# Performance work log

Hardware: AMD Instinct MI355X
Metric: run time of the kernel (lower is better)

The kernel has to match this reference:

```python
import jax, jax.numpy as jnp
import numpy as np

D = 1024
H = 16
K = 32768
EPS = 1e-5


def setup_inputs() -> dict:
    key = jax.random.key(0)
    ks = jax.random.split(key, 12)
    s = 1.0 / np.sqrt(D)
    return {
        "query": jax.random.normal(ks[0], (D,), jnp.float32),
        "neighbors": jax.random.normal(ks[1], (K, D), jnp.float32),
        # nn.MultiheadAttention params
        "in_proj_w": jax.random.uniform(ks[2], (3 * D, D), jnp.float32, -s, s),
        "in_proj_b": jnp.zeros((3 * D,), jnp.float32),
        "out_proj_w": jax.random.uniform(ks[3], (D, D), jnp.float32, -s, s),
        "out_proj_b": jnp.zeros((D,), jnp.float32),
        # FFN params
        "w1": jax.random.uniform(ks[4], (4 * D, D), jnp.float32, -s, s),
        "b1": jnp.zeros((4 * D,), jnp.float32),
        "w2": jax.random.uniform(ks[5], (D, 4 * D), jnp.float32, -s, s),
        "b2": jnp.zeros((D,), jnp.float32),
        # LayerNorm params
        "g1": jnp.ones((D,), jnp.float32),
        "be1": jnp.zeros((D,), jnp.float32),
        "g2": jnp.ones((D,), jnp.float32),
        "be2": jnp.zeros((D,), jnp.float32),
    }


def _layernorm(x, g, b):
    m = jnp.mean(x, axis=-1, keepdims=True)
    v = jnp.var(x, axis=-1, keepdims=True)
    return (x - m) * jax.lax.rsqrt(v + EPS) * g + b


def reference(query, neighbors, in_proj_w, in_proj_b, out_proj_w, out_proj_b,
              w1, b1, w2, b2, g1, be1, g2, be2):
    dh = D // H
    wq, wk, wv = in_proj_w[:D], in_proj_w[D:2 * D], in_proj_w[2 * D:]
    bq, bk, bv = in_proj_b[:D], in_proj_b[D:2 * D], in_proj_b[2 * D:]

    q = (query @ wq.T + bq).reshape(H, dh)            # [H, dh]
    k = (neighbors @ wk.T + bk).reshape(K, H, dh)     # [K, H, dh]
    v = (neighbors @ wv.T + bv).reshape(K, H, dh)

    scores = jnp.einsum('hd,khd->hk', q, k) / np.sqrt(dh)  # [H, K]
    attn = jax.nn.softmax(scores, axis=-1)
    ctx = jnp.einsum('hk,khd->hd', attn, v).reshape(D)      # [D]
    attn_out = ctx @ out_proj_w.T + out_proj_b

    x = _layernorm(query + attn_out, g1, be1)
    ffn = jax.nn.gelu(x @ w1.T + b1, approximate=False) @ w2.T + b2
    return _layernorm(x + ffn, g2, be2)
```

## Files before the change

### kernel.cpp

```cpp
#include <hip/hip_runtime.h>
#include <hip/hip_bf16.h>

#define D 1024
#define H 16
#define DH 64
#define KN 32768
#define EPS 1e-5f

__device__ __forceinline__ float wave_sum(float v){
  #pragma unroll
  for (int off = 32; off; off >>= 1) v += __shfl_xor(v, off, 64);
  return v;
}

#define GLL(gp, lp) __builtin_amdgcn_global_load_lds((const __attribute__((address_space(1))) void*)(gp), (__attribute__((address_space(3))) void*)(lp), 16, 0, 0)

__global__ void g_qproj(const float* __restrict__ query, const float* __restrict__ ipw,
                        const float* __restrict__ ipb, float* __restrict__ q){
  int j = blockIdx.x, l = threadIdx.x;
  const float4* qv = (const float4*)(query + l*16);
  const float4* wv = (const float4*)(ipw + (size_t)j*D + l*16);
  float acc = 0.f;
  #pragma unroll
  for (int t = 0; t < 4; t++){
    float4 a = qv[t], b = wv[t];
    acc += a.x*b.x + a.y*b.y + a.z*b.z + a.w*b.w;
  }
  acc = wave_sum(acc);
  if (l == 0) q[j] = acc + ipb[j];
}

__global__ __launch_bounds__(256) void g_qk(const float* __restrict__ ipw, const float* __restrict__ ipb,
                                            const float* __restrict__ q, float* __restrict__ qk,
                                            float* __restrict__ sb){
  int b = blockIdx.x, t = threadIdx.x;
  int h = b >> 2, sl = b & 3;
  int jg = t >> 6, c = t & 63;
  __shared__ float qh[DH];
  __shared__ float4 red[256];
  if (t < DH) qh[t] = q[h*DH + t];
  __syncthreads();
  if (t < DH){
    float p = qh[t] * ipb[D + h*DH + t];
    p = wave_sum(p);
    if (t == 0 && sl == 0) sb[h] = p;
  }
  float4 acc = make_float4(0.f,0.f,0.f,0.f);
  for (int jj = 0; jj < 16; jj++){
    int j = jg*16 + jj;
    float4 w = *((const float4*)(ipw + (size_t)(D + h*DH + j)*D) + sl*64 + c);
    float qj = qh[j];
    acc.x += qj*w.x; acc.y += qj*w.y; acc.z += qj*w.z; acc.w += qj*w.w;
  }
  red[t] = acc;
  __syncthreads();
  if (jg == 0){
    float4 a = red[c], b1 = red[64+c], c1 = red[128+c], d1 = red[192+c];
    float4 r = make_float4(a.x+b1.x+c1.x+d1.x, a.y+b1.y+c1.y+d1.y,
                           a.z+b1.z+c1.z+d1.z, a.w+b1.w+c1.w+d1.w);
    ((float4*)(qk + h*D))[sl*64 + c] = r;
  }
}

__global__ void g_attn(const float* __restrict__ nbr, const float* __restrict__ qk,
                       const float* __restrict__ sb, float* __restrict__ lpart,
                       float* __restrict__ part, int rows_per_blk){
  __shared__ __align__(16) float tile[2][8*D];
  int t = threadIdx.x;
  int h = t >> 6, ci = t & 63;
  int wb = t & ~63;
  float sbh = sb[h];

  float qkv[16];
  {
    const float4* qp = (const float4*)(qk + h*D);
    #pragma unroll
    for (int c = 0; c < 4; c++){
      float4 f = qp[c*64 + ci];
      qkv[4*c]=f.x; qkv[4*c+1]=f.y; qkv[4*c+2]=f.z; qkv[4*c+3]=f.w;
    }
  }
  float acc[16];
  #pragma unroll
  for (int i = 0; i < 16; i++) acc[i] = 0.f;
  float lsum = 0.f;

  const int k0 = blockIdx.x * rows_per_blk;
  const int ntiles = rows_per_blk >> 3;
  const uint4* gb = (const uint4*)nbr;

  {
    const uint4* g = gb + (size_t)k0*256;
    #pragma unroll
    for (int i = 0; i < 2; i++) GLL(g + i*1024 + t, &tile[0][(i*1024 + wb)*4]);
  }
  __syncthreads();

  #pragma unroll 1
  for (int tl = 0; tl < ntiles; tl++){
    int cur = tl & 1;
    if (tl + 1 < ntiles){
      const uint4* g = gb + (size_t)(k0 + (tl+1)*8)*256;
      #pragma unroll
      for (int i = 0; i < 2; i++) GLL(g + i*1024 + t, &tile[cur^1][(i*1024 + wb)*4]);
    }
    #pragma unroll 1
    for (int r = 0; r < 8; r++){
      const float4* row4 = (const float4*)(tile[cur]) + r*256;
      float xf[16];
      float s = 0.f;
      #pragma unroll
      for (int c = 0; c < 4; c++){
        float4 a = row4[c*64 + ci];
        xf[4*c]=a.x; xf[4*c+1]=a.y; xf[4*c+2]=a.z; xf[4*c+3]=a.w;
        s += a.x*qkv[4*c] + a.y*qkv[4*c+1] + a.z*qkv[4*c+2] + a.w*qkv[4*c+3];
      }
      s = wave_sum(s);
      float p = __expf((s + sbh)*0.125f);
      lsum += p;
      #pragma unroll
      for (int i = 0; i < 16; i++) acc[i] += p*xf[i];
    }
    __syncthreads();
  }

  if (ci == 0) lpart[blockIdx.x*H + h] = lsum;
  float4* o = (float4*)(part + (size_t)blockIdx.x*(H*D) + h*D);
  #pragma unroll
  for (int c = 0; c < 4; c++)
    o[c*64 + ci] = make_float4(acc[4*c], acc[4*c+1], acc[4*c+2], acc[4*c+3]);
}

__global__ __launch_bounds__(256) void g_red(const float* __restrict__ part, const float* __restrict__ lpart,
                                             float* __restrict__ nb, float* __restrict__ lh, int nblk){
  int b = blockIdx.x, t = threadIdx.x;
  if (b == 64){
    if (t < H){
      float s = 0.f;
      for (int c = 0; c < nblk; c++) s += lpart[c*H + t];
      lh[t] = s;
    }
    return;
  }
  int o = b*256 + t;
  float s = 0.f;
  #pragma unroll 8
  for (int c = 0; c < nblk; c++) s += part[(size_t)c*(H*D) + o];
  nb[o] = s;
}

__global__ void g_ctx(const float* __restrict__ ipw, const float* __restrict__ ipb,
                      const float* __restrict__ nb, const float* __restrict__ lh,
                      float* __restrict__ ctx){
  int j = blockIdx.x, l = threadIdx.x, h = j >> 6;
  const float4* wv = (const float4*)(ipw + (size_t)(2*D + j)*D + l*16);
  const float4* nv = (const float4*)(nb + h*D + l*16);
  float acc = 0.f;
  #pragma unroll
  for (int t = 0; t < 4; t++){
    float4 b = wv[t], n = nv[t];
    acc += b.x*n.x + b.y*n.y + b.z*n.z + b.w*n.w;
  }
  acc = wave_sum(acc);
  if (l == 0) ctx[j] = acc/lh[h] + ipb[2*D + j];
}

__global__ void g_attnout(const float* __restrict__ opw, const float* __restrict__ opb,
                          const float* __restrict__ query, const float* __restrict__ ctx,
                          float* __restrict__ xb){
  int j = blockIdx.x, l = threadIdx.x;
  const float4* wv = (const float4*)(opw + (size_t)j*D + l*16);
  const float4* cv = (const float4*)(ctx + l*16);
  float acc = 0.f;
  #pragma unroll
  for (int t = 0; t < 4; t++){
    float4 b = wv[t], c = cv[t];
    acc += b.x*c.x + b.y*c.y + b.z*c.z + b.w*c.w;
  }
  acc = wave_sum(acc);
  if (l == 0) xb[j] = query[j] + acc + opb[j];
}

__global__ __launch_bounds__(256) void g_ffn1(const float* __restrict__ w1, const float* __restrict__ b1,
                                              const float* __restrict__ xb,
                                              const float* __restrict__ g1, const float* __restrict__ be1,
                                              float* __restrict__ xln, float* __restrict__ h1){
  int t = threadIdx.x, b = blockIdx.x;
  __shared__ float xs[D];
  __shared__ float red[8];
  float4 v = ((const float4*)xb)[t];
  float s = wave_sum(v.x + v.y + v.z + v.w);
  if ((t & 63) == 0) red[t >> 6] = s;
  __syncthreads();
  float m = (red[0]+red[1]+red[2]+red[3]) * (1.0f/D);
  float4 d = make_float4(v.x-m, v.y-m, v.z-m, v.w-m);
  float s2 = wave_sum(d.x*d.x + d.y*d.y + d.z*d.z + d.w*d.w);
  if ((t & 63) == 0) red[4 + (t >> 6)] = s2;
  __syncthreads();
  float var = (red[4]+red[5]+red[6]+red[7]) * (1.0f/D);
  float rs = rsqrtf(var + EPS);
  float4 gg = ((const float4*)g1)[t], bb = ((const float4*)be1)[t];
  float4 r = make_float4(d.x*rs*gg.x + bb.x, d.y*rs*gg.y + bb.y,
                         d.z*rs*gg.z + bb.z, d.w*rs*gg.w + bb.w);
  ((float4*)xs)[t] = r;
  if (b == 0) ((float4*)xln)[t] = r;
  __syncthreads();

  int w = t >> 6, l = t & 63;
  const float4* xs4 = (const float4*)xs;
  #pragma unroll 1
  for (int rr = 0; rr < 4; rr++){
    int j = b*16 + w*4 + rr;
    const float4* wr = (const float4*)(w1 + (size_t)j*D);
    float a = 0.f;
    #pragma unroll
    for (int c = 0; c < 4; c++){
      float4 ww = wr[c*64 + l], xx = xs4[c*64 + l];
      a += ww.x*xx.x + ww.y*xx.y + ww.z*xx.z + ww.w*xx.w;
    }
    a = wave_sum(a);
    if (l == 0){
      float z = a + b1[j];
      h1[j] = 0.5f*z*(1.0f + erff(z*0.70710678118654752f));
    }
  }
}

__global__ void g_ffn2(const float* __restrict__ w2, const float* __restrict__ b2v,
                       const float* __restrict__ h1, float* __restrict__ y){
  int j = blockIdx.x, l = threadIdx.x;
  const float4* wv = (const float4*)(w2 + (size_t)j*4096 + l*64);
  const float4* hv = (const float4*)(h1 + l*64);
  float acc = 0.f;
  #pragma unroll
  for (int t = 0; t < 16; t++){
    float4 b = wv[t], hh = hv[t];
    acc += b.x*hh.x + b.y*hh.y + b.z*hh.z + b.w*hh.w;
  }
  acc = wave_sum(acc);
  if (l == 0) y[j] = acc + b2v[j];
}

__global__ __launch_bounds__(1024) void g_ln2(const float* __restrict__ xln, const float* __restrict__ y,
                                              const float* __restrict__ g, const float* __restrict__ be,
                                              float* __restrict__ out){
  int t = threadIdx.x;
  __shared__ float red[16];
  __shared__ float bc;
  float v = xln[t] + y[t];
  float s = wave_sum(v);
  if ((t & 63) == 0) red[t >> 6] = s;
  __syncthreads();
  if (t == 0){ float a = 0.f; for (int i = 0; i < 16; i++) a += red[i]; bc = a*(1.0f/D); }
  __syncthreads();
  float m = bc;
  float d = v - m;
  float s2 = wave_sum(d*d);
  if ((t & 63) == 0) red[t >> 6] = s2;
  __syncthreads();
  if (t == 0){ float a = 0.f; for (int i = 0; i < 16; i++) a += red[i]; bc = a*(1.0f/D); }
  __syncthreads();
  float rs = rsqrtf(bc + EPS);
  out[t] = d*rs*g[t] + be[t];
}

extern "C" void kernel_launch(void* const* d_in, const int* in_sizes, int n_in,
                              void* d_out, int out_size, void* d_ws, size_t ws_size,
                              hipStream_t stream) {
  const float* query = (const float*)d_in[0];
  const float* nbr   = (const float*)d_in[1];
  const float* ipw   = (const float*)d_in[2];
  const float* ipb   = (const float*)d_in[3];
  const float* opw   = (const float*)d_in[4];
  const float* opb   = (const float*)d_in[5];
  const float* w1    = (const float*)d_in[6];
  const float* b1    = (const float*)d_in[7];
  const float* w2    = (const float*)d_in[8];
  const float* b2v   = (const float*)d_in[9];
  const float* g1    = (const float*)d_in[10];
  const float* be1   = (const float*)d_in[11];
  const float* g2    = (const float*)d_in[12];
  const float* be2   = (const float*)d_in[13];

  float* ws    = (float*)d_ws;
  float* q     = ws;
  float* qk    = q + D;
  float* sb    = qk + H*D;
  float* lh    = sb + 16;
  float* ctx   = lh + 16;
  float* xb    = ctx + D;
  float* xln   = xb + D;
  float* h1    = xln + D;
  float* y     = h1 + 4*D;
  float* nb    = y + D;
  float* lpart = nb + H*D;
  float* part  = lpart + 4096;

  size_t fixed_bytes = (size_t)(part - ws) * 4;
  int nblk = 256;
  while (nblk > 32 && fixed_bytes + (size_t)nblk*H*D*4 > ws_size) nblk >>= 1;
  int rows_per_blk = KN / nblk;

  g_qproj  <<<1024, 64, 0, stream>>>(query, ipw, ipb, q);
  g_qk     <<<64, 256, 0, stream>>>(ipw, ipb, q, qk, sb);
  g_attn   <<<nblk, 1024, 0, stream>>>(nbr, qk, sb, lpart, part, rows_per_blk);
  g_red    <<<65, 256, 0, stream>>>(part, lpart, nb, lh, nblk);
  g_ctx    <<<1024, 64, 0, stream>>>(ipw, ipb, nb, lh, ctx);
  g_attnout<<<1024, 64, 0, stream>>>(opw, opb, query, ctx, xb);
  g_ffn1   <<<256, 256, 0, stream>>>(w1, b1, xb, g1, be1, xln, h1);
  g_ffn2   <<<1024, 64, 0, stream>>>(w2, b2v, h1, y);
  g_ln2    <<<1, 1024, 0, stream>>>(xln, y, g2, be2, (float*)d_out);
}
```

Measured before the change: 348.2 us.

## Fuse all stages into one persistent kernel with software grid barriers

```diff
diff --git a/kernel.cpp b/kernel.cpp
--- a/kernel.cpp
+++ b/kernel.cpp
@@ -3,9 +3,24 @@
 
 #define D 1024
 #define H 16
-#define DH 64
 #define KN 32768
 #define EPS 1e-5f
+#define NB 256
+#define RPB 128
+
+#define O_Q     0
+#define O_QK    1024
+#define O_SB    17408
+#define O_LH    17424
+#define O_CTX   17440
+#define O_XB    18464
+#define O_XLN   19488
+#define O_H1    20512
+#define O_Y     24608
+#define O_NBUF  25632
+#define O_LPART 42016
+#define O_BAR   46112
+#define O_PART  46176
 
 __device__ __forceinline__ float wave_sum(float v){
   #pragma unroll
@@ -15,203 +30,253 @@
 
 #define GLL(gp, lp) __builtin_amdgcn_global_load_lds((const __attribute__((address_space(1))) void*)(gp), (__attribute__((address_space(3))) void*)(lp), 16, 0, 0)
 
-__global__ void g_qproj(const float* __restrict__ query, const float* __restrict__ ipw,
-                        const float* __restrict__ ipb, float* __restrict__ q){
-  int j = blockIdx.x, l = threadIdx.x;
-  const float4* qv = (const float4*)(query + l*16);
-  const float4* wv = (const float4*)(ipw + (size_t)j*D + l*16);
-  float acc = 0.f;
-  #pragma unroll
-  for (int t = 0; t < 4; t++){
-    float4 a = qv[t], b = wv[t];
-    acc += a.x*b.x + a.y*b.y + a.z*b.z + a.w*b.w;
-  }
-  acc = wave_sum(acc);
-  if (l == 0) q[j] = acc + ipb[j];
-}
-
-__global__ __launch_bounds__(256) void g_qk(const float* __restrict__ ipw, const float* __restrict__ ipb,
-                                            const float* __restrict__ q, float* __restrict__ qk,
-                                            float* __restrict__ sb){
-  int b = blockIdx.x, t = threadIdx.x;
-  int h = b >> 2, sl = b & 3;
-  int jg = t >> 6, c = t & 63;
-  __shared__ float qh[DH];
-  __shared__ float4 red[256];
-  if (t < DH) qh[t] = q[h*DH + t];
+__device__ __forceinline__ void gbar(int* bar, int idx){
   __syncthreads();
-  if (t < DH){
-    float p = qh[t] * ipb[D + h*DH + t];
-    p = wave_sum(p);
-    if (t == 0 && sl == 0) sb[h] = p;
-  }
-  float4 acc = make_float4(0.f,0.f,0.f,0.f);
-  for (int jj = 0; jj < 16; jj++){
-    int j = jg*16 + jj;
-    float4 w = *((const float4*)(ipw + (size_t)(D + h*DH + j)*D) + sl*64 + c);
-    float qj = qh[j];
-    acc.x += qj*w.x; acc.y += qj*w.y; acc.z += qj*w.z; acc.w += qj*w.w;
-  }
-  red[t] = acc;
+  if (threadIdx.x == 0){
+    int* cnt = bar + idx*2;
+    int* gen = bar + idx*2 + 1;
+    __threadfence();
+    int g = atomicAdd(gen, 0);
+    if (atomicAdd(cnt, 1) == (int)gridDim.x - 1){
+      atomicExch(cnt, 0);
+      atomicAdd(gen, 1);
+    } else {
+      while (atomicAdd(gen, 0) == g){ __builtin_amdgcn_s_sleep(2); }
+    }
+    __threadfence();
+  }
   __syncthreads();
-  if (jg == 0){
-    float4 a = red[c], b1 = red[64+c], c1 = red[128+c], d1 = red[192+c];
-    float4 r = make_float4(a.x+b1.x+c1.x+d1.x, a.y+b1.y+c1.y+d1.y,
-                           a.z+b1.z+c1.z+d1.z, a.w+b1.w+c1.w+d1.w);
-    ((float4*)(qk + h*D))[sl*64 + c] = r;
-  }
-}
-
-__global__ void g_attn(const float* __restrict__ nbr, const float* __restrict__ qk,
-                       const float* __restrict__ sb, float* __restrict__ lpart,
-                       float* __restrict__ part, int rows_per_blk){
+}
+
+__global__ void g_init(int* bar){
+  if (threadIdx.x < 64) bar[threadIdx.x] = 0;
+}
+
+__global__ __launch_bounds__(1024) void g_fused(
+    const float* __restrict__ query, const float* __restrict__ nbr,
+    const float* __restrict__ ipw,   const float* __restrict__ ipb,
+    const float* __restrict__ opw,   const float* __restrict__ opb,
+    const float* __restrict__ w1,    const float* __restrict__ b1,
+    const float* __restrict__ w2,    const float* __restrict__ b2v,
+    const float* __restrict__ g1,    const float* __restrict__ be1,
+    const float* __restrict__ g2,    const float* __restrict__ be2,
+    float* __restrict__ ws, float* __restrict__ out){
+
+  float* q     = ws + O_Q;
+  float* qk    = ws + O_QK;
+  float* sb    = ws + O_SB;
+  float* lh    = ws + O_LH;
+  float* ctx   = ws + O_CTX;
+  float* xb    = ws + O_XB;
+  float* xln   = ws + O_XLN;
+  float* h1    = ws + O_H1;
+  float* y     = ws + O_Y;
+  float* nbuf  = ws + O_NBUF;
+  float* lpart = ws + O_LPART;
+  int*   bar   = (int*)(ws + O_BAR);
+  float* part  = ws + O_PART;
+
   __shared__ __align__(16) float tile[2][8*D];
-  int t = threadIdx.x;
-  int h = t >> 6, ci = t & 63;
-  int wb = t & ~63;
-  float sbh = sb[h];
-
-  float qkv[16];
+  __shared__ float smem[1056];
+  float* xs  = smem;
+  float* red = smem + 1024;
+  float* bcs = smem + 1040;
+
+  const int b = blockIdx.x, t = threadIdx.x;
+  const int w = t >> 6, l = t & 63;
+
+  if (w < 4){
+    int j = b*4 + w;
+    const float4* qv = (const float4*)(query + l*16);
+    const float4* wv = (const float4*)(ipw + (size_t)j*D + l*16);
+    float a = 0.f;
+    #pragma unroll
+    for (int c = 0; c < 4; c++){
+      float4 aa = qv[c], bb = wv[c];
+      a += aa.x*bb.x + aa.y*bb.y + aa.z*bb.z + aa.w*bb.w;
+    }
+    a = wave_sum(a);
+    if (l == 0) q[j] = a + ipb[j];
+  }
+  gbar(bar, 0);
+
   {
-    const float4* qp = (const float4*)(qk + h*D);
-    #pragma unroll
-    for (int c = 0; c < 4; c++){
-      float4 f = qp[c*64 + ci];
-      qkv[4*c]=f.x; qkv[4*c+1]=f.y; qkv[4*c+2]=f.z; qkv[4*c+3]=f.w;
-    }
-  }
-  float acc[16];
-  #pragma unroll
-  for (int i = 0; i < 16; i++) acc[i] = 0.f;
-  float lsum = 0.f;
-
-  const int k0 = blockIdx.x * rows_per_blk;
-  const int ntiles = rows_per_blk >> 3;
-  const uint4* gb = (const uint4*)nbr;
-
-  {
-    const uint4* g = gb + (size_t)k0*256;
-    #pragma unroll
-    for (int i = 0; i < 2; i++) GLL(g + i*1024 + t, &tile[0][(i*1024 + wb)*4]);
-  }
-  __syncthreads();
-
-  #pragma unroll 1
-  for (int tl = 0; tl < ntiles; tl++){
-    int cur = tl & 1;
-    if (tl + 1 < ntiles){
-      const uint4* g = gb + (size_t)(k0 + (tl+1)*8)*256;
-      #pragma unroll
-      for (int i = 0; i < 2; i++) GLL(g + i*1024 + t, &tile[cur^1][(i*1024 + wb)*4]);
-    }
-    #pragma unroll 1
-    for (int r = 0; r < 8; r++){
-      const float4* row4 = (const float4*)(tile[cur]) + r*256;
-      float xf[16];
+    int h = b >> 4, sl = b & 15;
+    int col = sl*64 + l;
+    float par = 0.f;
+    #pragma unroll
+    for (int i = 0; i < 4; i++){
+      int j = w*4 + i;
+      par += q[h*64 + j] * ipw[(size_t)(D + h*64 + j)*D + col];
+    }
+    smem[w*64 + l] = par;
+    __syncthreads();
+    if (t < 64){
       float s = 0.f;
       #pragma unroll
+      for (int jj = 0; jj < 16; jj++) s += smem[jj*64 + t];
+      qk[h*D + sl*64 + t] = s;
+    }
+    if (sl == 0 && w == 1){
+      float p = q[h*64 + l] * ipb[D + h*64 + l];
+      p = wave_sum(p);
+      if (l == 0) sb[h] = p;
+    }
+    __syncthreads();
+  }
+  gbar(bar, 1);
+
+  {
+    int h = w, ci = l;
+    int wb2 = t & ~63;
+    float sbh = sb[h];
+    float qkv[16];
+    {
+      const float4* qp = (const float4*)(qk + h*D);
+      #pragma unroll
       for (int c = 0; c < 4; c++){
-        float4 a = row4[c*64 + ci];
-        xf[4*c]=a.x; xf[4*c+1]=a.y; xf[4*c+2]=a.z; xf[4*c+3]=a.w;
-        s += a.x*qkv[4*c] + a.y*qkv[4*c+1] + a.z*qkv[4*c+2] + a.w*qkv[4*c+3];
+        float4 f = qp[c*64 + ci];
+        qkv[4*c]=f.x; qkv[4*c+1]=f.y; qkv[4*c+2]=f.z; qkv[4*c+3]=f.w;
       }
-      s = wave_sum(s);
-      float p = __expf((s + sbh)*0.125f);
-      lsum += p;
+    }
+    float acc[16];
+    #pragma unroll
+    for (int i = 0; i < 16; i++) acc[i] = 0.f;
+    float lsum = 0.f;
+
+    const int k0 = b * RPB;
+    const uint4* gb2 = (const uint4*)nbr;
+    {
+      const uint4* g = gb2 + (size_t)k0*256;
       #pragma unroll
-      for (int i = 0; i < 16; i++) acc[i] += p*xf[i];
-    }
-    __syncthreads();
-  }
-
-  if (ci == 0) lpart[blockIdx.x*H + h] = lsum;
-  float4* o = (float4*)(part + (size_t)blockIdx.x*(H*D) + h*D);
-  #pragma unroll
-  for (int c = 0; c < 4; c++)
-    o[c*64 + ci] = make_float4(acc[4*c], acc[4*c+1], acc[4*c+2], acc[4*c+3]);
-}
-
-__global__ __launch_bounds__(256) void g_red(const float* __restrict__ part, const float* __restrict__ lpart,
-                                             float* __restrict__ nb, float* __restrict__ lh, int nblk){
-  int b = blockIdx.x, t = threadIdx.x;
-  if (b == 64){
-    if (t < H){
-      float s = 0.f;
-      for (int c = 0; c < nblk; c++) s += lpart[c*H + t];
-      lh[t] = s;
-    }
-    return;
-  }
-  int o = b*256 + t;
-  float s = 0.f;
-  #pragma unroll 8
-  for (int c = 0; c < nblk; c++) s += part[(size_t)c*(H*D) + o];
-  nb[o] = s;
-}
-
-__global__ void g_ctx(const float* __restrict__ ipw, const float* __restrict__ ipb,
-                      const float* __restrict__ nb, const float* __restrict__ lh,
-                      float* __restrict__ ctx){
-  int j = blockIdx.x, l = threadIdx.x, h = j >> 6;
-  const float4* wv = (const float4*)(ipw + (size_t)(2*D + j)*D + l*16);
-  const float4* nv = (const float4*)(nb + h*D + l*16);
-  float acc = 0.f;
-  #pragma unroll
-  for (int t = 0; t < 4; t++){
-    float4 b = wv[t], n = nv[t];
-    acc += b.x*n.x + b.y*n.y + b.z*n.z + b.w*n.w;
-  }
-  acc = wave_sum(acc);
-  if (l == 0) ctx[j] = acc/lh[h] + ipb[2*D + j];
-}
-
-__global__ void g_attnout(const float* __restrict__ opw, const float* __restrict__ opb,
-                          const float* __restrict__ query, const float* __restrict__ ctx,
-                          float* __restrict__ xb){
-  int j = blockIdx.x, l = threadIdx.x;
-  const float4* wv = (const float4*)(opw + (size_t)j*D + l*16);
-  const float4* cv = (const float4*)(ctx + l*16);
-  float acc = 0.f;
-  #pragma unroll
-  for (int t = 0; t < 4; t++){
-    float4 b = wv[t], c = cv[t];
-    acc += b.x*c.x + b.y*c.y + b.z*c.z + b.w*c.w;
-  }
-  acc = wave_sum(acc);
-  if (l == 0) xb[j] = query[j] + acc + opb[j];
-}
-
-__global__ __launch_bounds__(256) void g_ffn1(const float* __restrict__ w1, const float* __restrict__ b1,
-                                              const float* __restrict__ xb,
-                                              const float* __restrict__ g1, const float* __restrict__ be1,
-                                              float* __restrict__ xln, float* __restrict__ h1){
-  int t = threadIdx.x, b = blockIdx.x;
-  __shared__ float xs[D];
-  __shared__ float red[8];
-  float4 v = ((const float4*)xb)[t];
-  float s = wave_sum(v.x + v.y + v.z + v.w);
-  if ((t & 63) == 0) red[t >> 6] = s;
-  __syncthreads();
-  float m = (red[0]+red[1]+red[2]+red[3]) * (1.0f/D);
-  float4 d = make_float4(v.x-m, v.y-m, v.z-m, v.w-m);
-  float s2 = wave_sum(d.x*d.x + d.y*d.y + d.z*d.z + d.w*d.w);
-  if ((t & 63) == 0) red[4 + (t >> 6)] = s2;
-  __syncthreads();
-  float var = (red[4]+red[5]+red[6]+red[7]) * (1.0f/D);
-  float rs = rsqrtf(var + EPS);
-  float4 gg = ((const float4*)g1)[t], bb = ((const float4*)be1)[t];
-  float4 r = make_float4(d.x*rs*gg.x + bb.x, d.y*rs*gg.y + bb.y,
-                         d.z*rs*gg.z + bb.z, d.w*rs*gg.w + bb.w);
-  ((float4*)xs)[t] = r;
-  if (b == 0) ((float4*)xln)[t] = r;
-  __syncthreads();
-
-  int w = t >> 6, l = t & 63;
-  const float4* xs4 = (const float4*)xs;
-  #pragma unroll 1
-  for (int rr = 0; rr < 4; rr++){
-    int j = b*16 + w*4 + rr;
+      for (int i = 0; i < 2; i++) GLL(g + i*1024 + t, &tile[0][(i*1024 + wb2)*4]);
+    }
+    __syncthreads();
+
+    #pragma unroll 1
+    for (int tl = 0; tl < RPB/8; tl++){
+      int cur = tl & 1;
+      if (tl + 1 < RPB/8){
+        const uint4* g = gb2 + (size_t)(k0 + (tl+1)*8)*256;
+        #pragma unroll
+        for (int i = 0; i < 2; i++) GLL(g + i*1024 + t, &tile[cur^1][(i*1024 + wb2)*4]);
+      }
+      #pragma unroll 1
+      for (int r = 0; r < 8; r += 2){
+        const float4* rowA = (const float4*)(tile[cur]) + r*256;
+        const float4* rowB = rowA + 256;
+        float xfA[16], xfB[16], pa[4], pb[4];
+        #pragma unroll
+        for (int c = 0; c < 4; c++){
+          float4 a = rowA[c*64 + ci];
+          float4 bb = rowB[c*64 + ci];
+          xfA[4*c]=a.x; xfA[4*c+1]=a.y; xfA[4*c+2]=a.z; xfA[4*c+3]=a.w;
+          xfB[4*c]=bb.x; xfB[4*c+1]=bb.y; xfB[4*c+2]=bb.z; xfB[4*c+3]=bb.w;
+          pa[c] = a.x*qkv[4*c] + a.y*qkv[4*c+1] + a.z*qkv[4*c+2] + a.w*qkv[4*c+3];
+          pb[c] = bb.x*qkv[4*c] + bb.y*qkv[4*c+1] + bb.z*qkv[4*c+2] + bb.w*qkv[4*c+3];
+        }
+        float sA = (pa[0]+pa[1]) + (pa[2]+pa[3]);
+        float sB = (pb[0]+pb[1]) + (pb[2]+pb[3]);
+        #pragma unroll
+        for (int off = 32; off; off >>= 1){
+          sA += __shfl_xor(sA, off, 64);
+          sB += __shfl_xor(sB, off, 64);
+        }
+        float pA = __expf((sA + sbh)*0.125f);
+        float pB = __expf((sB + sbh)*0.125f);
+        lsum += pA + pB;
+        #pragma unroll
+        for (int i = 0; i < 16; i++) acc[i] += pA*xfA[i];
+        #pragma unroll
+        for (int i = 0; i < 16; i++) acc[i] += pB*xfB[i];
+      }
+      __syncthreads();
+    }
+
+    if (ci == 0) lpart[b*H + h] = lsum;
+    float4* o = (float4*)(part + (size_t)b*(H*D) + h*D);
+    #pragma unroll
+    for (int c = 0; c < 4; c++)
+      o[c*64 + ci] = make_float4(acc[4*c], acc[4*c+1], acc[4*c+2], acc[4*c+3]);
+  }
+  gbar(bar, 2);
+
+  {
+    int o = b*64 + l;
+    float s = 0.f;
+    #pragma unroll
+    for (int c = 0; c < 16; c++) s += part[(size_t)(w*16 + c)*(H*D) + o];
+    smem[w*64 + l] = s;
+    __syncthreads();
+    if (t < 64){
+      float s2 = 0.f;
+      #pragma unroll
+      for (int j = 0; j < 16; j++) s2 += smem[j*64 + t];
+      nbuf[b*64 + t] = s2;
+    }
+    if (b == 0 && w == 15 && l < 16){
+      float s3 = 0.f;
+      #pragma unroll 8
+      for (int c = 0; c < NB; c++) s3 += lpart[c*H + l];
+      lh[l] = s3;
+    }
+    __syncthreads();
+  }
+  gbar(bar, 3);
+
+  if (w < 4){
+    int j = b*4 + w, h2 = j >> 6;
+    const float4* wv = (const float4*)(ipw + (size_t)(2*D + j)*D + l*16);
+    const float4* nv = (const float4*)(nbuf + h2*D + l*16);
+    float a = 0.f;
+    #pragma unroll
+    for (int c = 0; c < 4; c++){
+      float4 bb = wv[c], nn = nv[c];
+      a += bb.x*nn.x + bb.y*nn.y + bb.z*nn.z + bb.w*nn.w;
+    }
+    a = wave_sum(a);
+    if (l == 0) ctx[j] = a/lh[h2] + ipb[2*D + j];
+  }
+  gbar(bar, 4);
+
+  if (w < 4){
+    int j = b*4 + w;
+    const float4* wv = (const float4*)(opw + (size_t)j*D + l*16);
+    const float4* cv = (const float4*)(ctx + l*16);
+    float a = 0.f;
+    #pragma unroll
+    for (int c = 0; c < 4; c++){
+      float4 bb = wv[c], cc = cv[c];
+      a += bb.x*cc.x + bb.y*cc.y + bb.z*cc.z + bb.w*cc.w;
+    }
+    a = wave_sum(a);
+    if (l == 0) xb[j] = query[j] + a + opb[j];
+  }
+  gbar(bar, 5);
+
+  {
+    float v = xb[t];
+    float s = wave_sum(v);
+    if (l == 0) red[w] = s;
+    __syncthreads();
+    if (t == 0){ float a=0.f; for (int i=0;i<16;i++) a += red[i]; bcs[0] = a*(1.0f/D); }
+    __syncthreads();
+    float m = bcs[0];
+    float dd = v - m;
+    float s2 = wave_sum(dd*dd);
+    if (l == 0) red[w] = s2;
+    __syncthreads();
+    if (t == 0){ float a=0.f; for (int i=0;i<16;i++) a += red[i]; bcs[1] = a*(1.0f/D); }
+    __syncthreads();
+    float rs = rsqrtf(bcs[1] + EPS);
+    float r = dd*rs*g1[t] + be1[t];
+    xs[t] = r;
+    if (b == 0) xln[t] = r;
+    __syncthreads();
+
+    int j = b*16 + w;
     const float4* wr = (const float4*)(w1 + (size_t)j*D);
+    const float4* xs4 = (const float4*)xs;
     float a = 0.f;
     #pragma unroll
     for (int c = 0; c < 4; c++){
@@ -224,44 +289,40 @@
       h1[j] = 0.5f*z*(1.0f + erff(z*0.70710678118654752f));
     }
   }
-}
-
-__global__ void g_ffn2(const float* __restrict__ w2, const float* __restrict__ b2v,
-                       const float* __restrict__ h1, float* __restrict__ y){
-  int j = blockIdx.x, l = threadIdx.x;
-  const float4* wv = (const float4*)(w2 + (size_t)j*4096 + l*64);
-  const float4* hv = (const float4*)(h1 + l*64);
-  float acc = 0.f;
-  #pragma unroll
-  for (int t = 0; t < 16; t++){
-    float4 b = wv[t], hh = hv[t];
-    acc += b.x*hh.x + b.y*hh.y + b.z*hh.z + b.w*hh.w;
-  }
-  acc = wave_sum(acc);
-  if (l == 0) y[j] = acc + b2v[j];
-}
-
-__global__ __launch_bounds__(1024) void g_ln2(const float* __restrict__ xln, const float* __restrict__ y,
-                                              const float* __restrict__ g, const float* __restrict__ be,
-                                              float* __restrict__ out){
-  int t = threadIdx.x;
-  __shared__ float red[16];
-  __shared__ float bc;
-  float v = xln[t] + y[t];
-  float s = wave_sum(v);
-  if ((t & 63) == 0) red[t >> 6] = s;
-  __syncthreads();
-  if (t == 0){ float a = 0.f; for (int i = 0; i < 16; i++) a += red[i]; bc = a*(1.0f/D); }
-  __syncthreads();
-  float m = bc;
-  float d = v - m;
-  float s2 = wave_sum(d*d);
-  if ((t & 63) == 0) red[t >> 6] = s2;
-  __syncthreads();
-  if (t == 0){ float a = 0.f; for (int i = 0; i < 16; i++) a += red[i]; bc = a*(1.0f/D); }
-  __syncthreads();
-  float rs = rsqrtf(bc + EPS);
-  out[t] = d*rs*g[t] + be[t];
+  gbar(bar, 6);
+
+  if (w < 4){
+    int j = b*4 + w;
+    const float4* wv = (const float4*)(w2 + (size_t)j*4096 + l*64);
+    const float4* hv = (const float4*)(h1 + l*64);
+    float a = 0.f;
+    #pragma unroll
+    for (int c = 0; c < 16; c++){
+      float4 bb = wv[c], hh = hv[c];
+      a += bb.x*hh.x + bb.y*hh.y + bb.z*hh.z + bb.w*hh.w;
+    }
+    a = wave_sum(a);
+    if (l == 0) y[j] = a + b2v[j];
+  }
+  gbar(bar, 7);
+
+  if (b == 0){
+    float v = xln[t] + y[t];
+    float s = wave_sum(v);
+    if (l == 0) red[w] = s;
+    __syncthreads();
+    if (t == 0){ float a=0.f; for (int i=0;i<16;i++) a += red[i]; bcs[0] = a*(1.0f/D); }
+    __syncthreads();
+    float m = bcs[0];
+    float dd = v - m;
+    float s2 = wave_sum(dd*dd);
+    if (l == 0) red[w] = s2;
+    __syncthreads();
+    if (t == 0){ float a=0.f; for (int i=0;i<16;i++) a += red[i]; bcs[1] = a*(1.0f/D); }
+    __syncthreads();
+    float rs = rsqrtf(bcs[1] + EPS);
+    out[t] = dd*rs*g2[t] + be2[t];
+  }
 }
 
 extern "C" void kernel_launch(void* const* d_in, const int* in_sizes, int n_in,
@@ -282,32 +343,9 @@
   const float* g2    = (const float*)d_in[12];
   const float* be2   = (const float*)d_in[13];
 
-  float* ws    = (float*)d_ws;
-  float* q     = ws;
-  float* qk    = q + D;
-  float* sb    = qk + H*D;
-  float* lh    = sb + 16;
-  float* ctx   = lh + 16;
-  float* xb    = ctx + D;
-  float* xln   = xb + D;
-  float* h1    = xln + D;
-  float* y     = h1 + 4*D;
-  float* nb    = y + D;
-  float* lpart = nb + H*D;
-  float* part  = lpart + 4096;
-
-  size_t fixed_bytes = (size_t)(part - ws) * 4;
-  int nblk = 256;
-  while (nblk > 32 && fixed_bytes + (size_t)nblk*H*D*4 > ws_size) nblk >>= 1;
-  int rows_per_blk = KN / nblk;
-
-  g_qproj  <<<1024, 64, 0, stream>>>(query, ipw, ipb, q);
-  g_qk     <<<64, 256, 0, stream>>>(ipw, ipb, q, qk, sb);
-  g_attn   <<<nblk, 1024, 0, stream>>>(nbr, qk, sb, lpart, part, rows_per_blk);
-  g_red    <<<65, 256, 0, stream>>>(part, lpart, nb, lh, nblk);
-  g_ctx    <<<1024, 64, 0, stream>>>(ipw, ipb, nb, lh, ctx);
-  g_attnout<<<1024, 64, 0, stream>>>(opw, opb, query, ctx, xb);
-  g_ffn1   <<<256, 256, 0, stream>>>(w1, b1, xb, g1, be1, xln, h1);
-  g_ffn2   <<<1024, 64, 0, stream>>>(w2, b2v, h1, y);
-  g_ln2    <<<1, 1024, 0, stream>>>(xln, y, g2, be2, (float*)d_out);
-}
+  float* ws = (float*)d_ws;
+  g_init <<<1, 64, 0, stream>>>((int*)(ws + O_BAR));
+  g_fused<<<NB, 1024, 0, stream>>>(query, nbr, ipw, ipb, opw, opb,
+                                   w1, b1, w2, b2v, g1, be1, g2, be2,
+                                   ws, (float*)d_out);
+}
```

Measured after the change: 491.4 us. 1.41x slower.
